# Kernel tuning notes

Measured on AMD Instinct MI355X. Metric: run time of the kernel, lower is better.

The kernel has to match this reference:

```python
import jax, jax.numpy as jnp
import numpy as np

B, H, W, C, S, ITERS = 32, 80, 80, 32, 9, 3
HW = H * W
SCALE = C ** -0.5


def _grid(h, w):
    # matches SoftPositionEmbedding.build_grid: [1, h, w, 4] = [g, 1-g]
    r = jnp.stack(jnp.meshgrid(jnp.linspace(0., 1., h), jnp.linspace(0., 1., w), indexing='ij'), -1)
    return jnp.concatenate([r, 1. - r], -1)[None].astype(jnp.float32)


def _ln(x, g, b, ax):
    m = x.mean(ax, keepdims=True)
    v = x.var(ax, keepdims=True)
    return (x - m) / jnp.sqrt(v + 1e-5) * g + b


def _conv(x, w, b, p):
    y = jax.lax.conv_general_dilated(x, w, (1, 1), [(p, p), (p, p)],
                                     dimension_numbers=('NCHW', 'OIHW', 'NCHW'))
    return y + b[None, :, None, None]


def _convT(x, w, b, p):
    # stride-1 ConvTranspose2d == conv with spatially flipped kernel, pad k-1-p; w is [I,O,kh,kw]
    k = w.shape[-1]
    q = k - 1 - p
    y = jax.lax.conv_general_dilated(x, jnp.flip(w, (2, 3)), (1, 1), [(q, q), (q, q)],
                                     dimension_numbers=('NCHW', 'IOHW', 'NCHW'))
    return y + b[None, :, None, None]


def setup_inputs() -> dict:
    key = jax.random.key(0)
    ks = iter(jax.random.split(key, 64))

    def n(sh, s=0.05):
        return jax.random.normal(next(ks), sh, jnp.float32) * s

    return dict(
        x=jax.random.normal(next(ks), (B, 1, H, W), jnp.float32),
        slot_noise=jax.random.normal(next(ks), (B, S, C), jnp.float32),
        enc_w1=n((C, 1, 5, 5)), enc_b1=jnp.zeros((C,)),
        enc_w2=n((C, C, 5, 5)), enc_b2=jnp.zeros((C,)),
        enc_w3=n((C, C, 5, 5)), enc_b3=jnp.zeros((C,)),
        enc_w4=n((C, C, 5, 5)), enc_b4=jnp.zeros((C,)),
        pe_enc_w=n((C, 4)), pe_enc_b=jnp.zeros((C,)),
        ln_enc_g=jnp.ones((HW, C)), ln_enc_b=jnp.zeros((HW, C)),
        mlp_w1=n((C, C)), mlp_b1=jnp.zeros((C,)),
        mlp_w2=n((C, C)), mlp_b2=jnp.zeros((C,)),
        slots_mu=n((1, 1, C), 1.0), slots_sigma=jnp.abs(n((1, 1, C), 1.0)),
        ni_g=jnp.ones((C,)), ni_b=jnp.zeros((C,)),
        ns_g=jnp.ones((C,)), ns_b=jnp.zeros((C,)),
        q_w=n((C, C)), q_b=jnp.zeros((C,)),
        k_w=n((C, C)), k_b=jnp.zeros((C,)),
        v_w=n((C, C)), v_b=jnp.zeros((C,)),
        gru_wih=n((3 * C, C)), gru_whh=n((3 * C, C)),
        gru_bih=jnp.zeros((3 * C,)), gru_bhh=jnp.zeros((3 * C,)),
        res_ln_g=jnp.ones((C,)), res_ln_b=jnp.zeros((C,)),
        res_w1=n((C, C)), res_b1=jnp.zeros((C,)),
        res_w2=n((C, C)), res_b2=jnp.zeros((C,)),
        pe_dec_w=n((C, 4)), pe_dec_b=jnp.zeros((C,)),
        dec_w1=n((C, C, 5, 5)), dec_b1=jnp.zeros((C,)),
        dec_w2=n((C, C, 5, 5)), dec_b2=jnp.zeros((C,)),
        dec_w3=n((C, C, 5, 5)), dec_b3=jnp.zeros((C,)),
        dec_w4=n((C, 2, 3, 3)), dec_b4=jnp.zeros((2,)),
    )


def _forward(x, slot_noise, enc_w1, enc_b1, enc_w2, enc_b2, enc_w3, enc_b3, enc_w4, enc_b4,
             pe_enc_w, pe_enc_b, ln_enc_g, ln_enc_b, mlp_w1, mlp_b1, mlp_w2, mlp_b2,
             slots_mu, slots_sigma, ni_g, ni_b, ns_g, ns_b, q_w, q_b, k_w, k_b, v_w, v_b,
             gru_wih, gru_whh, gru_bih, gru_bhh, res_ln_g, res_ln_b, res_w1, res_b1,
             res_w2, res_b2, pe_dec_w, pe_dec_b, dec_w1, dec_b1, dec_w2, dec_b2,
             dec_w3, dec_b3, dec_w4, dec_b4):
    grid = _grid(H, W)  # [1,H,W,4]
    # --- conv encoder ---
    h = jax.nn.relu(_conv(x, enc_w1, enc_b1, 2))
    h = jax.nn.relu(_conv(h, enc_w2, enc_b2, 2))
    h = jax.nn.relu(_conv(h, enc_w3, enc_b3, 2))
    h = jax.nn.relu(_conv(h, enc_w4, enc_b4, 2))
    h = h.transpose(0, 2, 3, 1) + (grid @ pe_enc_w.T + pe_enc_b)  # soft pos emb
    h = h.reshape(B, HW, C)
    h = _ln(h, ln_enc_g, ln_enc_b, (-2, -1))  # LayerNorm([HW, C]): joint over last 2 dims
    h = jax.nn.relu(h @ mlp_w1.T + mlp_b1) @ mlp_w2.T + mlp_b2
    # --- slot attention ---
    slots = slots_mu + slots_sigma * slot_noise  # torch.normal(mu, sigma)
    xn = _ln(h, ni_g, ni_b, -1)
    keys = xn @ k_w.T + k_b
    values = xn @ v_w.T + v_b
    attn = None
    for _ in range(ITERS):
        prev = slots
        sn = _ln(slots, ns_g, ns_b, -1)
        q = sn @ q_w.T + q_b
        dots = jnp.einsum('bid,bjd->bij', q, keys) * SCALE  # [B,S,HW]
        attn = jax.nn.softmax(dots, axis=1) + 1e-8  # softmax over slots
        attn = attn / attn.sum(-1, keepdims=True)
        upd = jnp.einsum('bjd,bij->bid', values, attn)  # [B,S,C]
        # PyTorch GRUCell
        u2 = upd.reshape(-1, C)
        h2 = prev.reshape(-1, C)
        gx = u2 @ gru_wih.T + gru_bih
        gh = h2 @ gru_whh.T + gru_bhh
        xr, xz, xc = jnp.split(gx, 3, -1)
        hr, hz, hc = jnp.split(gh, 3, -1)
        r = jax.nn.sigmoid(xr + hr)
        z = jax.nn.sigmoid(xz + hz)
        cand = jnp.tanh(xc + r * hc)
        slots = ((1. - z) * cand + z * h2).reshape(B, S, C)
        res = _ln(slots, res_ln_g, res_ln_b, -1)
        res = jax.nn.relu(res @ res_w1.T + res_b1) @ res_w2.T + res_b2
        slots = slots + res
    # --- spatial-broadcast decoder ---
    d = jnp.broadcast_to(slots.reshape(B * S, 1, 1, C), (B * S, H, W, C))
    d = d + (grid @ pe_dec_w.T + pe_dec_b)
    d = d.transpose(0, 3, 1, 2)
    d = jax.nn.relu(_convT(d, dec_w1, dec_b1, 2))
    d = jax.nn.relu(_convT(d, dec_w2, dec_b2, 2))
    d = jax.nn.relu(_convT(d, dec_w3, dec_b3, 2))
    d = _convT(d, dec_w4, dec_b4, 1)
    d = d.transpose(0, 2, 3, 1).reshape(B, S, H, W, 2)
    recon, mlog = d[..., :1], d[..., 1:]
    mask = jax.nn.softmax(mlog, axis=1)  # over slots
    combined = (recon * mask).sum(1).transpose(0, 3, 1, 2)  # [B,1,H,W]
    return (combined, recon.transpose(0, 1, 4, 2, 3), mask.transpose(0, 1, 4, 2, 3),
            slots, attn.reshape(B, S, 1, H, W))


def reference(x, slot_noise, enc_w1, enc_b1, enc_w2, enc_b2, enc_w3, enc_b3, enc_w4, enc_b4,
              pe_enc_w, pe_enc_b, ln_enc_g, ln_enc_b, mlp_w1, mlp_b1, mlp_w2, mlp_b2,
              slots_mu, slots_sigma, ni_g, ni_b, ns_g, ns_b, q_w, q_b, k_w, k_b, v_w, v_b,
              gru_wih, gru_whh, gru_bih, gru_bhh, res_ln_g, res_ln_b, res_w1, res_b1,
              res_w2, res_b2, pe_dec_w, pe_dec_b, dec_w1, dec_b1, dec_w2, dec_b2,
              dec_w3, dec_b3, dec_w4, dec_b4):
    return _forward(x, slot_noise, enc_w1, enc_b1, enc_w2, enc_b2, enc_w3, enc_b3, enc_w4, enc_b4,
                    pe_enc_w, pe_enc_b, ln_enc_g, ln_enc_b, mlp_w1, mlp_b1, mlp_w2, mlp_b2,
                    slots_mu, slots_sigma, ni_g, ni_b, ns_g, ns_b, q_w, q_b, k_w, k_b, v_w, v_b,
                    gru_wih, gru_whh, gru_bih, gru_bhh, res_ln_g, res_ln_b, res_w1, res_b1,
                    res_w2, res_b2, pe_dec_w, pe_dec_b, dec_w1, dec_b1, dec_w2, dec_b2,
                    dec_w3, dec_b3, dec_w4, dec_b4)
```

## Files before the change

kernel.cpp:

```cpp
#include <hip/hip_runtime.h>
#include <cstddef>
#include <cstdint>


namespace {

constexpr int Bb  = 32;
constexpr int HWp = 6400;
constexpr float SCALEf = 0.17677669529663687f;

constexpr size_t O_COMB  = 0;
constexpr size_t O_RECON = 204800;
constexpr size_t O_MASK  = 2048000;
constexpr size_t O_SLOTS = 3891200;
constexpr size_t O_ATTN  = 3900416;

constexpr size_t W_PEENC = 0;
constexpr size_t W_PEDEC = 204800;
constexpr size_t W_BASE  = 409600;
constexpr size_t W_TC    = 512000;
constexpr size_t W_TS    = 537600;
constexpr size_t W_WP    = 768000;
constexpr size_t W_LNPART= 844800;
constexpr size_t W_MEANR = 846400;
constexpr size_t W_Q     = 846464;
constexpr size_t W_SLOTS = 855680;
constexpr size_t W_APART = 864896;
constexpr size_t W_RSUM  = 872096;
constexpr size_t W_UP2   = 872384;
constexpr size_t W_KEYS  = 1102784;
constexpr size_t W_VALS  = 4379584;
constexpr size_t W_POOL  = 7656384;
constexpr size_t W_TOTAL = 29115328;

typedef __attribute__((ext_vector_type(8))) short short8;
typedef __attribute__((ext_vector_type(4))) float f32x4;

__device__ __forceinline__ ushort f2bf(float f) {
  uint u = __builtin_bit_cast(uint, f);
  uint r = (u + 0x7fffu + ((u >> 16) & 1u)) >> 16;
  return (ushort)r;
}
__device__ __forceinline__ float bf2f(ushort b) {
  uint u = ((uint)b) << 16;
  return __builtin_bit_cast(float, u);
}
__device__ __forceinline__ void unpk2(uint w, float& a, float& b) {
  a = __builtin_bit_cast(float, w << 16);
  b = __builtin_bit_cast(float, w & 0xffff0000u);
}

__device__ __forceinline__ void ln32v(const float* x, const float* __restrict__ g,
                                      const float* __restrict__ b, float* y) {
  float m = 0.f;
#pragma unroll
  for (int c = 0; c < 32; ++c) m += x[c];
  m *= (1.f / 32.f);
  float v = 0.f;
#pragma unroll
  for (int c = 0; c < 32; ++c) { float d = x[c] - m; v += d * d; }
  v *= (1.f / 32.f);
  float rs = rsqrtf(v + 1e-5f);
#pragma unroll
  for (int c = 0; c < 32; ++c) y[c] = (x[c] - m) * rs * g[c] + b[c];
}

__device__ __forceinline__ void matvec32(const float* __restrict__ W,
                                         const float* __restrict__ bias,
                                         const float* x, float* y, bool relu) {
#pragma unroll
  for (int o = 0; o < 32; ++o) {
    float a = bias[o];
#pragma unroll
    for (int c = 0; c < 32; ++c) a = fmaf(x[c], W[o * 32 + c], a);
    y[o] = relu ? fmaxf(a, 0.f) : a;
  }
}

__device__ __forceinline__ float lane_ln(float v, int o, const float* __restrict__ g,
                                         const float* __restrict__ b) {
  float s = v;
#pragma unroll
  for (int m = 16; m >= 1; m >>= 1) s += __shfl_xor(s, m);
  float mean = s * (1.f / 32.f);
  float d = v - mean;
  float q = d * d;
#pragma unroll
  for (int m = 16; m >= 1; m >>= 1) q += __shfl_xor(q, m);
  float rstd = rsqrtf(q * (1.f / 32.f) + 1e-5f);
  return d * rstd * g[o] + b[o];
}


__global__ void k_pe_maps(const float* __restrict__ pew_e, const float* __restrict__ peb_e,
                          const float* __restrict__ pew_d, const float* __restrict__ peb_d,
                          float* __restrict__ pe_enc, float* __restrict__ pe_dec) {
  int hw = blockIdx.x * 256 + threadIdx.x;
  if (hw >= HWp) return;
  int y = hw / 80, x = hw % 80;
  float g0 = y * (1.f / 79.f), g1 = x * (1.f / 79.f);
  float g2 = 1.f - g0, g3 = 1.f - g1;
#pragma unroll
  for (int c = 0; c < 32; ++c) {
    pe_enc[(size_t)hw * 32 + c] = peb_e[c] + g0 * pew_e[c * 4] + g1 * pew_e[c * 4 + 1] +
                                  g2 * pew_e[c * 4 + 2] + g3 * pew_e[c * 4 + 3];
    pe_dec[(size_t)c * HWp + hw] = peb_d[c] + g0 * pew_d[c * 4] + g1 * pew_d[c * 4 + 1] +
                                   g2 * pew_d[c * 4 + 2] + g3 * pew_d[c * 4 + 3];
  }
}


__global__ void k_pack(const float* __restrict__ w, ushort* __restrict__ dst, int trans) {
  int tap = blockIdx.x;
  int grp = threadIdx.x >> 6, lane = threadIdx.x & 63;
  int ky = tap / 5, kx = tap % 5;
  int m = grp * 16 + (lane & 15);
  int kb = (lane >> 4) * 8;
  ushort* o = dst + ((size_t)(tap * 2 + grp) * 64 + lane) * 8;
#pragma unroll
  for (int j = 0; j < 8; ++j) {
    int k = kb + j;
    float v = trans ? w[(size_t)k * 800 + m * 25 + (4 - ky) * 5 + (4 - kx)]
                    : w[(size_t)m * 800 + k * 25 + ky * 5 + kx];
    o[j] = f2bf(v);
  }
}


__global__ void k_prep_tc(const float* __restrict__ w, float* __restrict__ tc) {
  const int rep[5] = {0, 1, 40, 78, 79};
  int cls = blockIdx.x;
  int yc = cls / 5, xc = cls % 5;
  int ci = threadIdx.x >> 5, co = threadIdx.x & 31;
  int yr = rep[yc], xr = rep[xc];
  float s = 0.f;
#pragma unroll
  for (int ky = 0; ky < 5; ++ky) {
    if ((unsigned)(yr + ky - 2) >= 80u) continue;
#pragma unroll
    for (int kx = 0; kx < 5; ++kx) {
      if ((unsigned)(xr + kx - 2) >= 80u) continue;
      s += w[(size_t)ci * 800 + co * 25 + (4 - ky) * 5 + (4 - kx)];
    }
  }
  tc[(size_t)cls * 1024 + ci * 32 + co] = s;
}

__global__ void k_ts(const float* __restrict__ tc, const float* __restrict__ slots,
                     float* __restrict__ ts) {
  int idx = blockIdx.x * 256 + threadIdx.x;
  if (idx >= 288 * 800) return;
  int img = idx / 800, rem = idx % 800;
  int cls = rem >> 5, o = rem & 31;
  float s = 0.f;
#pragma unroll
  for (int ci = 0; ci < 32; ++ci)
    s += tc[(size_t)cls * 1024 + ci * 32 + o] * slots[(size_t)img * 32 + ci];
  ts[idx] = s;
}


template <int MODE, bool RELU>
__global__ __launch_bounds__(256, 2) void k_conv_mfma(
    const void* __restrict__ in_, const ushort* __restrict__ wp,
    const float* __restrict__ bias, ushort* __restrict__ out_,
    const float* __restrict__ ts, int n0) {
  __shared__ int4 sm[4032];
  const int n = blockIdx.y, rt = blockIdx.x;
  const int t = threadIdx.x;

  for (int i = t; i < 4032; i += 256) {
    int x = i % 84, ru = i / 84;
    int r = ru >> 2, u = ru & 3;
    int gy = rt * 8 + r - 2, gx = x - 2;
    int4 pk = {0, 0, 0, 0};
    if ((unsigned)gy < 80u && (unsigned)gx < 80u) {
      int hw = gy * 80 + gx;
      if constexpr (MODE == 0) {
        const float* fp = (const float*)in_;
        ushort bb[8];
#pragma unroll
        for (int j = 0; j < 8; ++j)
          bb[j] = f2bf(fp[(size_t)(u * 8 + j) * HWp + hw]);
        pk.x = (int)((uint)bb[0] | ((uint)bb[1] << 16));
        pk.y = (int)((uint)bb[2] | ((uint)bb[3] << 16));
        pk.z = (int)((uint)bb[4] | ((uint)bb[5] << 16));
        pk.w = (int)((uint)bb[6] | ((uint)bb[7] << 16));
      } else if constexpr (MODE == 1) {
        pk = *(const int4*)((const ushort*)in_ + ((size_t)n * HWp + hw) * 32 + u * 8);
      } else {
        int4 bp = *(const int4*)((const ushort*)in_ + (size_t)hw * 32 + u * 8);
        int yc = gy < 2 ? gy : (gy > 77 ? gy - 75 : 2);
        int xc = gx < 2 ? gx : (gx > 77 ? gx - 75 : 2);
        const float* tp = ts + ((size_t)(n0 + n) * 25 + (yc * 5 + xc)) * 32 + u * 8;
        float t0, t1;
        uint* pw = (uint*)&pk;
        const uint* bw = (const uint*)&bp;
#pragma unroll
        for (int h = 0; h < 4; ++h) {
          unpk2(bw[h], t0, t1);
          float f0 = fmaxf(t0 + tp[2 * h], 0.f);
          float f1 = fmaxf(t1 + tp[2 * h + 1], 0.f);
          pw[h] = (uint)f2bf(f0) | ((uint)f2bf(f1) << 16);
        }
      }
    }
    int up = u ^ ((x >> 1) & 3);
    sm[(r * 84 + x) * 4 + up] = pk;
  }
  __syncthreads();

  const int wv = t >> 6, lane = t & 63;
  const int l15 = lane & 15, lg = lane >> 4;
  const short8* smS = (const short8*)sm;

  f32x4 acc[2][5][2];
#pragma unroll
  for (int a = 0; a < 2; ++a)
#pragma unroll
    for (int b = 0; b < 5; ++b)
#pragma unroll
      for (int c = 0; c < 2; ++c) acc[a][b][c] = f32x4{0.f, 0.f, 0.f, 0.f};

  for (int dy = 0; dy < 5; ++dy) {
    for (int dx = 0; dx < 5; ++dx) {
      int tap = dy * 5 + dx;
      short8 A0 = *(const short8*)(wp + ((size_t)(tap * 2 + 0) * 64 + lane) * 8);
      short8 A1 = *(const short8*)(wp + ((size_t)(tap * 2 + 1) * 64 + lane) * 8);
#pragma unroll
      for (int ri = 0; ri < 2; ++ri) {
        int rbase = (wv * 2 + ri + dy) * 336;
#pragma unroll
        for (int xg = 0; xg < 5; ++xg) {
          int xs = xg * 16 + l15 + dx;
          short8 Bv = smS[rbase + xs * 4 + (lg ^ ((xs >> 1) & 3))];
          acc[ri][xg][0] = __builtin_amdgcn_mfma_f32_16x16x32_bf16(A0, Bv, acc[ri][xg][0], 0, 0, 0);
          acc[ri][xg][1] = __builtin_amdgcn_mfma_f32_16x16x32_bf16(A1, Bv, acc[ri][xg][1], 0, 0, 0);
        }
      }
    }
  }

  float bv[2][4];
#pragma unroll
  for (int cg = 0; cg < 2; ++cg)
#pragma unroll
    for (int q = 0; q < 4; ++q) bv[cg][q] = bias[cg * 16 + lg * 4 + q];
  int y0 = rt * 8 + wv * 2;
#pragma unroll
  for (int ri = 0; ri < 2; ++ri) {
#pragma unroll
    for (int xg = 0; xg < 5; ++xg) {
      size_t px = (size_t)n * HWp + (y0 + ri) * 80 + (xg * 16 + l15);
#pragma unroll
      for (int cg = 0; cg < 2; ++cg) {
        f32x4 v = acc[ri][xg][cg];
        float o0 = v[0] + bv[cg][0], o1 = v[1] + bv[cg][1];
        float o2 = v[2] + bv[cg][2], o3 = v[3] + bv[cg][3];
        if (RELU) {
          o0 = fmaxf(o0, 0.f); o1 = fmaxf(o1, 0.f);
          o2 = fmaxf(o2, 0.f); o3 = fmaxf(o3, 0.f);
        }
        uint2 pk;
        pk.x = (uint)f2bf(o0) | ((uint)f2bf(o1) << 16);
        pk.y = (uint)f2bf(o2) | ((uint)f2bf(o3) << 16);
        *(uint2*)(out_ + px * 32 + cg * 16 + lg * 4) = pk;
      }
    }
  }
}


__global__ __launch_bounds__(256) void k_conv1(const float* __restrict__ in,
                                               const float* __restrict__ w,
                                               const float* __restrict__ b,
                                               ushort* __restrict__ out) {
  int hw = blockIdx.x * 256 + threadIdx.x;
  int n = blockIdx.y;
  int y = hw / 80, x = hw % 80;
  float xv[25];
#pragma unroll
  for (int ky = 0; ky < 5; ++ky)
#pragma unroll
    for (int kx = 0; kx < 5; ++kx) {
      int iy = y + ky - 2, ix = x + kx - 2;
      xv[ky * 5 + kx] = ((unsigned)iy < 80u && (unsigned)ix < 80u)
                            ? in[(size_t)n * HWp + iy * 80 + ix] : 0.f;
    }
  float a[32];
#pragma unroll
  for (int co = 0; co < 32; ++co) {
    float s = b[co];
#pragma unroll
    for (int tp = 0; tp < 25; ++tp) s = fmaf(xv[tp], w[co * 25 + tp], s);
    a[co] = fmaxf(s, 0.f);
  }
  ushort* op = out + ((size_t)n * HWp + hw) * 32;
#pragma unroll
  for (int g = 0; g < 4; ++g) {
    uint4 pk;
    pk.x = (uint)f2bf(a[g * 8 + 0]) | ((uint)f2bf(a[g * 8 + 1]) << 16);
    pk.y = (uint)f2bf(a[g * 8 + 2]) | ((uint)f2bf(a[g * 8 + 3]) << 16);
    pk.z = (uint)f2bf(a[g * 8 + 4]) | ((uint)f2bf(a[g * 8 + 5]) << 16);
    pk.w = (uint)f2bf(a[g * 8 + 6]) | ((uint)f2bf(a[g * 8 + 7]) << 16);
    *(uint4*)(op + g * 8) = pk;
  }
}


__global__ __launch_bounds__(256) void k_conv4(const ushort* __restrict__ in,
                                               const float* __restrict__ w,
                                               const float* __restrict__ b,
                                               float* __restrict__ outR,
                                               float* __restrict__ outM, int n0) {
  __shared__ float sw[2 * 288];
  for (int e = threadIdx.x; e < 576; e += 256) {
    int co = e / 288, rem = e % 288;
    int tap = rem / 32, ci = rem % 32;
    sw[e] = w[(size_t)(ci * 2 + co) * 9 + 8 - tap];
  }
  __syncthreads();
  int hw = blockIdx.x * 256 + threadIdx.x;
  int nl = blockIdx.y;
  int y = hw / 80, x = hw % 80;
  float a0 = b[0], a1 = b[1];
  const ushort* ip = in + (size_t)nl * HWp * 32;
#pragma unroll
  for (int ky = 0; ky < 3; ++ky) {
#pragma unroll
    for (int kx = 0; kx < 3; ++kx) {
      int iy = y + ky - 1, ix = x + kx - 1;
      if ((unsigned)iy >= 80u || (unsigned)ix >= 80u) continue;
      int tap = ky * 3 + kx;
      const int4* p = (const int4*)(ip + (size_t)(iy * 80 + ix) * 32);
      const float* w0 = sw + tap * 32;
      const float* w1 = sw + 288 + tap * 32;
#pragma unroll
      for (int u = 0; u < 4; ++u) {
        int4 ch = p[u];
        const uint* cw = (const uint*)&ch;
#pragma unroll
        for (int h = 0; h < 4; ++h) {
          float v0, v1;
          unpk2(cw[h], v0, v1);
          int ci = u * 8 + h * 2;
          a0 = fmaf(v0, w0[ci], a0);     a1 = fmaf(v0, w1[ci], a1);
          a0 = fmaf(v1, w0[ci + 1], a0); a1 = fmaf(v1, w1[ci + 1], a1);
        }
      }
    }
  }
  outR[(size_t)(n0 + nl) * HWp + hw] = a0;
  outM[(size_t)(n0 + nl) * HWp + hw] = a1;
}


__global__ __launch_bounds__(256) void k_hstats(const ushort* __restrict__ enc,
                                                const float* __restrict__ pe_enc,
                                                float* __restrict__ lnpart) {
  int b = blockIdx.y;
  int hw = blockIdx.x * 256 + threadIdx.x;
  const int4* ep = (const int4*)(enc + ((size_t)b * HWp + hw) * 32);
  float v[32];
#pragma unroll
  for (int u = 0; u < 4; ++u) {
    int4 ch = ep[u];
    const uint* cw = (const uint*)&ch;
#pragma unroll
    for (int h = 0; h < 4; ++h) unpk2(cw[h], v[u * 8 + h * 2], v[u * 8 + h * 2 + 1]);
  }
  float s = 0.f, ss = 0.f;
#pragma unroll
  for (int c = 0; c < 32; ++c) {
    v[c] += pe_enc[(size_t)hw * 32 + c];
    s += v[c]; ss += v[c] * v[c];
  }
  __shared__ float r1[256], r2[256];
  r1[threadIdx.x] = s; r2[threadIdx.x] = ss;
  __syncthreads();
  for (int off = 128; off > 0; off >>= 1) {
    if (threadIdx.x < off) { r1[threadIdx.x] += r1[threadIdx.x + off]; r2[threadIdx.x] += r2[threadIdx.x + off]; }
    __syncthreads();
  }
  if (threadIdx.x == 0) {
    lnpart[(size_t)(b * 25 + blockIdx.x) * 2] = r1[0];
    lnpart[(size_t)(b * 25 + blockIdx.x) * 2 + 1] = r2[0];
  }
}

__global__ void k_statsfin(const float* __restrict__ lnpart, float* __restrict__ meanr) {
  int b = threadIdx.x;
  if (b >= 32) return;
  float s = 0.f, ss = 0.f;
  for (int k = 0; k < 25; ++k) {
    s += lnpart[(size_t)(b * 25 + k) * 2];
    ss += lnpart[(size_t)(b * 25 + k) * 2 + 1];
  }
  float m = s * (1.f / 204800.f);
  float var = ss * (1.f / 204800.f) - m * m;
  meanr[b * 2] = m;
  meanr[b * 2 + 1] = rsqrtf(var + 1e-5f);
}


__global__ __launch_bounds__(256) void k_lnmlpkv(
    const ushort* __restrict__ enc, const float* __restrict__ pe_enc,
    const float* __restrict__ meanr,
    const float* __restrict__ g, const float* __restrict__ bb,
    const float* __restrict__ w1, const float* __restrict__ b1,
    const float* __restrict__ w2, const float* __restrict__ b2,
    const float* __restrict__ nig, const float* __restrict__ nib,
    const float* __restrict__ kw, const float* __restrict__ kb,
    const float* __restrict__ vw, const float* __restrict__ vb,
    ushort* __restrict__ keys, ushort* __restrict__ vals) {
  int b = blockIdx.y;
  int hw = blockIdx.x * 256 + threadIdx.x;
  float x[32], t0[32], t1[32];
  const int4* ep = (const int4*)(enc + ((size_t)b * HWp + hw) * 32);
#pragma unroll
  for (int u = 0; u < 4; ++u) {
    int4 ch = ep[u];
    const uint* cw = (const uint*)&ch;
#pragma unroll
    for (int h = 0; h < 4; ++h) unpk2(cw[h], x[u * 8 + h * 2], x[u * 8 + h * 2 + 1]);
  }
  float m = meanr[b * 2], rs = meanr[b * 2 + 1];
#pragma unroll
  for (int c = 0; c < 32; ++c) {
    float h = x[c] + pe_enc[(size_t)hw * 32 + c];
    x[c] = (h - m) * rs * g[(size_t)hw * 32 + c] + bb[(size_t)hw * 32 + c];
  }
  matvec32(w1, b1, x, t0, true);
  matvec32(w2, b2, t0, t1, false);
  ln32v(t1, nig, nib, x);
  matvec32(kw, kb, x, t0, false);
  matvec32(vw, vb, x, t1, false);
  ushort* kp = keys + ((size_t)b * HWp + hw) * 32;
  ushort* vp = vals + ((size_t)b * HWp + hw) * 32;
#pragma unroll
  for (int gq = 0; gq < 4; ++gq) {
    uint4 pk, pv;
    pk.x = (uint)f2bf(t0[gq * 8 + 0]) | ((uint)f2bf(t0[gq * 8 + 1]) << 16);
    pk.y = (uint)f2bf(t0[gq * 8 + 2]) | ((uint)f2bf(t0[gq * 8 + 3]) << 16);
    pk.z = (uint)f2bf(t0[gq * 8 + 4]) | ((uint)f2bf(t0[gq * 8 + 5]) << 16);
    pk.w = (uint)f2bf(t0[gq * 8 + 6]) | ((uint)f2bf(t0[gq * 8 + 7]) << 16);
    pv.x = (uint)f2bf(t1[gq * 8 + 0]) | ((uint)f2bf(t1[gq * 8 + 1]) << 16);
    pv.y = (uint)f2bf(t1[gq * 8 + 2]) | ((uint)f2bf(t1[gq * 8 + 3]) << 16);
    pv.z = (uint)f2bf(t1[gq * 8 + 4]) | ((uint)f2bf(t1[gq * 8 + 5]) << 16);
    pv.w = (uint)f2bf(t1[gq * 8 + 6]) | ((uint)f2bf(t1[gq * 8 + 7]) << 16);
    *(uint4*)(kp + gq * 8) = pk;
    *(uint4*)(vp + gq * 8) = pv;
  }
}


__global__ __launch_bounds__(256) void k_init_q(
    const float* __restrict__ mu, const float* __restrict__ sig,
    const float* __restrict__ noise,
    const float* __restrict__ nsg, const float* __restrict__ nsb,
    const float* __restrict__ qw, const float* __restrict__ qb,
    float* __restrict__ slots, float* __restrict__ qbuf) {
  int rl = threadIdx.x >> 5, o = threadIdx.x & 31;
  int r = blockIdx.x * 8 + rl;
  float s = mu[o] + sig[o] * noise[(size_t)r * 32 + o];
  slots[(size_t)r * 32 + o] = s;
  float y = lane_ln(s, o, nsg, nsb);
  __shared__ float S[8][32];
  S[rl][o] = y;
  __syncthreads();
  float qv = qb[o];
#pragma unroll
  for (int c = 0; c < 32; ++c) qv = fmaf(S[rl][c], qw[o * 32 + c], qv);
  qbuf[(size_t)r * 32 + o] = qv;
}

template <bool LAST>
__global__ __launch_bounds__(256) void k_dots_upd(
    const float* __restrict__ qbuf, const ushort* __restrict__ keys,
    const ushort* __restrict__ vals, float* __restrict__ attnt,
    float* __restrict__ apart, float* __restrict__ up2) {
  int b = blockIdx.y, jb = blockIdx.x;
  int t = threadIdx.x;
  int j = jb * 256 + t;
  __shared__ float qs[288];
  __shared__ float aL[2304];
  __shared__ float wr[36];
  for (int e = t; e < 288; e += 256) qs[e] = qbuf[(size_t)b * 288 + e];
  __syncthreads();
  float k[32];
  const int4* kp = (const int4*)(keys + ((size_t)b * HWp + j) * 32);
#pragma unroll
  for (int u = 0; u < 4; ++u) {
    int4 ch = kp[u];
    const uint* cw = (const uint*)&ch;
#pragma unroll
    for (int h = 0; h < 4; ++h) unpk2(cw[h], k[u * 8 + h * 2], k[u * 8 + h * 2 + 1]);
  }
  float d[9];
#pragma unroll
  for (int i = 0; i < 9; ++i) {
    float a = 0.f;
#pragma unroll
    for (int c = 0; c < 32; ++c) a = fmaf(qs[i * 32 + c], k[c], a);
    d[i] = a * SCALEf;
  }
  float mx = d[0];
#pragma unroll
  for (int i = 1; i < 9; ++i) mx = fmaxf(mx, d[i]);
  float sum = 0.f;
#pragma unroll
  for (int i = 0; i < 9; ++i) { d[i] = __expf(d[i] - mx); sum += d[i]; }
  float inv = 1.f / sum;
  float a9[9];
#pragma unroll
  for (int i = 0; i < 9; ++i) {
    a9[i] = d[i] * inv + 1e-8f;
    if (LAST) attnt[((size_t)b * 9 + i) * HWp + j] = a9[i];
    aL[t * 9 + i] = a9[i];
  }
  int lane = t & 63, wid = t >> 6;
#pragma unroll
  for (int i = 0; i < 9; ++i) {
    float v = a9[i];
    for (int off = 32; off > 0; off >>= 1) v += __shfl_down(v, off);
    if (lane == 0) wr[wid * 9 + i] = v;
  }
  __syncthreads();
  if (t < 9)
    apart[(size_t)(b * 9 + t) * 25 + jb] = wr[t] + wr[9 + t] + wr[18 + t] + wr[27 + t];
  int c = t & 31, g = t >> 5;
  float acc[9];
#pragma unroll
  for (int i = 0; i < 9; ++i) acc[i] = 0.f;
  const ushort* vp = vals + ((size_t)b * HWp + jb * 256) * 32 + c;
  for (int jj = g; jj < 256; jj += 8) {
    float v = bf2f(vp[(size_t)jj * 32]);
#pragma unroll
    for (int i = 0; i < 9; ++i) acc[i] = fmaf(v, aL[jj * 9 + i], acc[i]);
  }
  __syncthreads();
#pragma unroll
  for (int i = 0; i < 9; ++i) aL[(i * 8 + g) * 32 + c] = acc[i];
  __syncthreads();
  for (int i = g; i < 9; i += 8) {
    float s = 0.f;
#pragma unroll
    for (int g2 = 0; g2 < 8; ++g2) s += aL[(i * 8 + g2) * 32 + c];
    up2[(((size_t)b * 25 + jb) * 9 + i) * 32 + c] = s;
  }
}

__global__ __launch_bounds__(256) void k_gru_fused(
    const float* __restrict__ up2, const float* __restrict__ apart,
    float* __restrict__ slots, float* __restrict__ rowsum, float* __restrict__ qbuf,
    const float* __restrict__ wih, const float* __restrict__ whh,
    const float* __restrict__ bih, const float* __restrict__ bhh,
    const float* __restrict__ rlg, const float* __restrict__ rlb,
    const float* __restrict__ rw1, const float* __restrict__ rb1,
    const float* __restrict__ rw2, const float* __restrict__ rb2,
    const float* __restrict__ nsg, const float* __restrict__ nsb,
    const float* __restrict__ qw, const float* __restrict__ qb) {
  int rl = threadIdx.x >> 5, o = threadIdx.x & 31;
  int r = blockIdx.x * 8 + rl;
  int b = r / 9, i = r - b * 9;

  float rs = 0.f;
#pragma unroll
  for (int k = 0; k < 25; ++k) rs += apart[(size_t)(b * 9 + i) * 25 + k];
  if (o == 0) rowsum[r] = rs;

  float uo = 0.f;
#pragma unroll
  for (int jc = 0; jc < 25; ++jc) uo += up2[(((size_t)b * 25 + jc) * 9 + i) * 32 + o];
  uo /= rs;
  float ho = slots[(size_t)r * 32 + o];

  __shared__ float Us[8][32], Hs[8][32];
  Us[rl][o] = uo; Hs[rl][o] = ho;
  __syncthreads();

  float xr = bih[o], xz = bih[32 + o], xc = bih[64 + o];
  float hr = bhh[o], hz = bhh[32 + o], hc = bhh[64 + o];
#pragma unroll
  for (int c = 0; c < 32; ++c) {
    float u = Us[rl][c], h = Hs[rl][c];
    xr = fmaf(u, wih[o * 32 + c], xr);          hr = fmaf(h, whh[o * 32 + c], hr);
    xz = fmaf(u, wih[(32 + o) * 32 + c], xz);   hz = fmaf(h, whh[(32 + o) * 32 + c], hz);
    xc = fmaf(u, wih[(64 + o) * 32 + c], xc);   hc = fmaf(h, whh[(64 + o) * 32 + c], hc);
  }
  float rr = 1.f / (1.f + __expf(-(xr + hr)));
  float zz = 1.f / (1.f + __expf(-(xz + hz)));
  float cand = tanhf(xc + rr * hc);
  float sm = (1.f - zz) * cand + zz * ho;

  float y = lane_ln(sm, o, rlg, rlb);
  __syncthreads();
  Us[rl][o] = y;
  __syncthreads();
  float t1 = rb1[o];
#pragma unroll
  for (int c = 0; c < 32; ++c) t1 = fmaf(Us[rl][c], rw1[o * 32 + c], t1);
  t1 = fmaxf(t1, 0.f);
  Hs[rl][o] = t1;
  __syncthreads();
  float res = rb2[o];
#pragma unroll
  for (int c = 0; c < 32; ++c) res = fmaf(Hs[rl][c], rw2[o * 32 + c], res);
  float ns = sm + res;
  slots[(size_t)r * 32 + o] = ns;

  float y2 = lane_ln(ns, o, nsg, nsb);
  __syncthreads();
  Us[rl][o] = y2;
  __syncthreads();
  float qv = qb[o];
#pragma unroll
  for (int c = 0; c < 32; ++c) qv = fmaf(Us[rl][c], qw[o * 32 + c], qv);
  qbuf[(size_t)r * 32 + o] = qv;
}


__global__ void k_attn_out(const float* __restrict__ attnt, const float* __restrict__ rsum,
                           float* __restrict__ out) {
  size_t idx = (size_t)blockIdx.x * 256 + threadIdx.x;
  out[O_ATTN + idx] = attnt[idx] / rsum[idx / HWp];
}

__global__ void k_slots_out(const float* __restrict__ slots, float* __restrict__ out) {
  int idx = blockIdx.x * 256 + threadIdx.x;
  if (idx < 9216) out[O_SLOTS + idx] = slots[idx];
}

__global__ __launch_bounds__(256) void k_final(float* __restrict__ out) {
  int b = blockIdx.y;
  int j = blockIdx.x * 256 + threadIdx.x;
  float r[9], ml[9];
#pragma unroll
  for (int s = 0; s < 9; ++s) {
    r[s]  = out[O_RECON + (size_t)(b * 9 + s) * HWp + j];
    ml[s] = out[O_MASK  + (size_t)(b * 9 + s) * HWp + j];
  }
  float mx = ml[0];
#pragma unroll
  for (int s = 1; s < 9; ++s) mx = fmaxf(mx, ml[s]);
  float sum = 0.f;
#pragma unroll
  for (int s = 0; s < 9; ++s) { ml[s] = __expf(ml[s] - mx); sum += ml[s]; }
  float inv = 1.f / sum;
  float comb = 0.f;
#pragma unroll
  for (int s = 0; s < 9; ++s) {
    float mk = ml[s] * inv;
    comb = fmaf(r[s], mk, comb);
    out[O_MASK + (size_t)(b * 9 + s) * HWp + j] = mk;
  }
  out[O_COMB + (size_t)b * HWp + j] = comb;
}

}


extern "C" void kernel_launch(void* const* d_in, const int* in_sizes, int n_in,
                              void* d_out, int out_size, void* d_ws, size_t ws_size,
                              hipStream_t stream) {
  if (ws_size < W_TOTAL * sizeof(float)) return;

  const float* in_x       = (const float*)d_in[0];
  const float* slot_noise = (const float*)d_in[1];
  const float* enc_w1 = (const float*)d_in[2];   const float* enc_b1 = (const float*)d_in[3];
  const float* enc_w2 = (const float*)d_in[4];   const float* enc_b2 = (const float*)d_in[5];
  const float* enc_w3 = (const float*)d_in[6];   const float* enc_b3 = (const float*)d_in[7];
  const float* enc_w4 = (const float*)d_in[8];   const float* enc_b4 = (const float*)d_in[9];
  const float* pe_enc_w = (const float*)d_in[10]; const float* pe_enc_b = (const float*)d_in[11];
  const float* ln_enc_g = (const float*)d_in[12]; const float* ln_enc_b = (const float*)d_in[13];
  const float* mlp_w1 = (const float*)d_in[14];  const float* mlp_b1 = (const float*)d_in[15];
  const float* mlp_w2 = (const float*)d_in[16];  const float* mlp_b2 = (const float*)d_in[17];
  const float* slots_mu = (const float*)d_in[18]; const float* slots_sigma = (const float*)d_in[19];
  const float* ni_g = (const float*)d_in[20];    const float* ni_b = (const float*)d_in[21];
  const float* ns_g = (const float*)d_in[22];    const float* ns_b = (const float*)d_in[23];
  const float* q_w = (const float*)d_in[24];     const float* q_b = (const float*)d_in[25];
  const float* k_w = (const float*)d_in[26];     const float* k_b = (const float*)d_in[27];
  const float* v_w = (const float*)d_in[28];     const float* v_b = (const float*)d_in[29];
  const float* gru_wih = (const float*)d_in[30]; const float* gru_whh = (const float*)d_in[31];
  const float* gru_bih = (const float*)d_in[32]; const float* gru_bhh = (const float*)d_in[33];
  const float* res_ln_g = (const float*)d_in[34]; const float* res_ln_b = (const float*)d_in[35];
  const float* res_w1 = (const float*)d_in[36];  const float* res_b1 = (const float*)d_in[37];
  const float* res_w2 = (const float*)d_in[38];  const float* res_b2 = (const float*)d_in[39];
  const float* pe_dec_w = (const float*)d_in[40]; const float* pe_dec_b = (const float*)d_in[41];
  const float* dec_w1 = (const float*)d_in[42];  const float* dec_b1 = (const float*)d_in[43];
  const float* dec_w2 = (const float*)d_in[44];  const float* dec_b2 = (const float*)d_in[45];
  const float* dec_w3 = (const float*)d_in[46];  const float* dec_b3 = (const float*)d_in[47];
  const float* dec_w4 = (const float*)d_in[48];  const float* dec_b4 = (const float*)d_in[49];

  float* ws  = (float*)d_ws;
  float* out = (float*)d_out;
  ushort* wp = (ushort*)(ws + W_WP);

  k_pe_maps<<<dim3(25), 256, 0, stream>>>(pe_enc_w, pe_enc_b, pe_dec_w, pe_dec_b,
                                          ws + W_PEENC, ws + W_PEDEC);

  const size_t WPSTR = 25 * 2 * 64 * 8;
  k_pack<<<dim3(25), 128, 0, stream>>>(enc_w2, wp + 0 * WPSTR, 0);
  k_pack<<<dim3(25), 128, 0, stream>>>(enc_w3, wp + 1 * WPSTR, 0);
  k_pack<<<dim3(25), 128, 0, stream>>>(enc_w4, wp + 2 * WPSTR, 0);
  k_pack<<<dim3(25), 128, 0, stream>>>(dec_w1, wp + 3 * WPSTR, 1);
  k_pack<<<dim3(25), 128, 0, stream>>>(dec_w2, wp + 4 * WPSTR, 1);
  k_pack<<<dim3(25), 128, 0, stream>>>(dec_w3, wp + 5 * WPSTR, 1);
  k_prep_tc<<<dim3(25), 1024, 0, stream>>>(dec_w1, ws + W_TC);

  ushort* base  = (ushort*)(ws + W_BASE);
  ushort* keys  = (ushort*)(ws + W_KEYS);
  ushort* vals  = (ushort*)(ws + W_VALS);
  float*  attnt = ws + W_POOL;
  ushort* E1    = (ushort*)(ws + W_POOL);
  ushort* E2    = (ushort*)(ws + W_POOL + 3276800);

  k_conv_mfma<0, false><<<dim3(10, 1), 256, 0, stream>>>(
      ws + W_PEDEC, wp + 3 * WPSTR, dec_b1, base, nullptr, 0);

  k_conv1<<<dim3(25, Bb), 256, 0, stream>>>(in_x, enc_w1, enc_b1, E1);
  k_conv_mfma<1, true><<<dim3(10, Bb), 256, 0, stream>>>(E1, wp + 0 * WPSTR, enc_b2, E2, nullptr, 0);
  k_conv_mfma<1, true><<<dim3(10, Bb), 256, 0, stream>>>(E2, wp + 1 * WPSTR, enc_b3, E1, nullptr, 0);
  k_conv_mfma<1, true><<<dim3(10, Bb), 256, 0, stream>>>(E1, wp + 2 * WPSTR, enc_b4, E2, nullptr, 0);

  k_hstats<<<dim3(25, Bb), 256, 0, stream>>>(E2, ws + W_PEENC, ws + W_LNPART);
  k_statsfin<<<dim3(1), 64, 0, stream>>>(ws + W_LNPART, ws + W_MEANR);
  k_lnmlpkv<<<dim3(25, Bb), 256, 0, stream>>>(E2, ws + W_PEENC, ws + W_MEANR,
                                              ln_enc_g, ln_enc_b,
                                              mlp_w1, mlp_b1, mlp_w2, mlp_b2,
                                              ni_g, ni_b, k_w, k_b, v_w, v_b,
                                              keys, vals);

  k_init_q<<<dim3(36), 256, 0, stream>>>(slots_mu, slots_sigma, slot_noise,
                                         ns_g, ns_b, q_w, q_b, ws + W_SLOTS, ws + W_Q);
  for (int it = 0; it < 3; ++it) {
    if (it == 2)
      k_dots_upd<true><<<dim3(25, Bb), 256, 0, stream>>>(ws + W_Q, keys, vals, attnt,
                                                         ws + W_APART, ws + W_UP2);
    else
      k_dots_upd<false><<<dim3(25, Bb), 256, 0, stream>>>(ws + W_Q, keys, vals, attnt,
                                                          ws + W_APART, ws + W_UP2);
    k_gru_fused<<<dim3(36), 256, 0, stream>>>(ws + W_UP2, ws + W_APART,
                                              ws + W_SLOTS, ws + W_RSUM, ws + W_Q,
                                              gru_wih, gru_whh, gru_bih, gru_bhh,
                                              res_ln_g, res_ln_b, res_w1, res_b1,
                                              res_w2, res_b2, ns_g, ns_b, q_w, q_b);
  }
  k_attn_out<<<dim3(7200), 256, 0, stream>>>(attnt, ws + W_RSUM, out);
  k_slots_out<<<dim3(36), 256, 0, stream>>>(ws + W_SLOTS, out);

  k_ts<<<dim3(900), 256, 0, stream>>>(ws + W_TC, ws + W_SLOTS, ws + W_TS);

  ushort* XA = (ushort*)(ws + W_POOL);
  ushort* XB = XA + (size_t)96 * 32 * HWp;
  for (int ch = 0; ch < 3; ++ch) {
    int n0 = ch * 96;
    k_conv_mfma<2, true><<<dim3(10, 96), 256, 0, stream>>>(base, wp + 4 * WPSTR, dec_b2, XA,
                                                           ws + W_TS, n0);
    k_conv_mfma<1, true><<<dim3(10, 96), 256, 0, stream>>>(XA, wp + 5 * WPSTR, dec_b3, XB,
                                                           nullptr, 0);
    k_conv4<<<dim3(25, 96), 256, 0, stream>>>(XB, dec_w4, dec_b4,
                                              out + O_RECON, out + O_MASK, n0);
  }

  k_final<<<dim3(25, Bb), 256, 0, stream>>>(out);
}
```

Baseline: 696.9 us.

## Run encoder LN+MLP+K/V projection on MFMA bf16 matrix cores

Replaces the per-thread scalar fp32 matvec chain (MLP two layers, LayerNorm, K and V projections) with bf16 MFMA 16x16x32 ops. The four 32x32 weights are pre-packed into MFMA fragment layout, and intermediates go through swizzled LDS to re-layout between layers. LayerNorm is done with cross-lane shuffles. This cuts the heavy scalar FMA and register cost of the old kernel. The tradeoff is extra bf16 rounding of intermediate activations.

```diff
diff --git a/kernel.cpp b/kernel.cpp
--- a/kernel.cpp
+++ b/kernel.cpp
@@ -21,16 +21,17 @@
 constexpr size_t W_TC    = 512000;
 constexpr size_t W_TS    = 537600;
 constexpr size_t W_WP    = 768000;
-constexpr size_t W_LNPART= 844800;
-constexpr size_t W_MEANR = 846400;
-constexpr size_t W_Q     = 846464;
-constexpr size_t W_SLOTS = 855680;
-constexpr size_t W_APART = 864896;
-constexpr size_t W_RSUM  = 872096;
-constexpr size_t W_UP2   = 872384;
-constexpr size_t W_KEYS  = 1102784;
-constexpr size_t W_VALS  = 4379584;
-constexpr size_t W_POOL  = 7656384;
+constexpr size_t W_WPM   = 844800;
+constexpr size_t W_LNPART= 846848;
+constexpr size_t W_MEANR = 848448;
+constexpr size_t W_Q     = 848512;
+constexpr size_t W_SLOTS = 857728;
+constexpr size_t W_APART = 866944;
+constexpr size_t W_RSUM  = 874144;
+constexpr size_t W_UP2   = 874432;
+constexpr size_t W_KEYS  = 1104832;
+constexpr size_t W_VALS  = 4381632;
+constexpr size_t W_POOL  = 7658432;
 constexpr size_t W_TOTAL = 29115328;
 
 typedef __attribute__((ext_vector_type(8))) short short8;
@@ -48,21 +49,6 @@
 __device__ __forceinline__ void unpk2(uint w, float& a, float& b) {
   a = __builtin_bit_cast(float, w << 16);
   b = __builtin_bit_cast(float, w & 0xffff0000u);
-}
-
-__device__ __forceinline__ void ln32v(const float* x, const float* __restrict__ g,
-                                      const float* __restrict__ b, float* y) {
-  float m = 0.f;
-#pragma unroll
-  for (int c = 0; c < 32; ++c) m += x[c];
-  m *= (1.f / 32.f);
-  float v = 0.f;
-#pragma unroll
-  for (int c = 0; c < 32; ++c) { float d = x[c] - m; v += d * d; }
-  v *= (1.f / 32.f);
-  float rs = rsqrtf(v + 1e-5f);
-#pragma unroll
-  for (int c = 0; c < 32; ++c) y[c] = (x[c] - m) * rs * g[c] + b[c];
 }
 
 __device__ __forceinline__ void matvec32(const float* __restrict__ W,
@@ -124,6 +110,14 @@
                     : w[(size_t)m * 800 + k * 25 + ky * 5 + kx];
     o[j] = f2bf(v);
   }
+}
+
+__global__ void k_pack_mat(const float* __restrict__ w, ushort* __restrict__ dst) {
+  int grp = threadIdx.x >> 6, lane = threadIdx.x & 63;
+  int m = grp * 16 + (lane & 15), kb = (lane >> 4) * 8;
+  ushort* o = dst + ((size_t)(grp * 64 + lane)) * 8;
+#pragma unroll
+  for (int j = 0; j < 8; ++j) o[j] = f2bf(w[m * 32 + kb + j]);
 }
 
 
@@ -403,53 +397,155 @@
 }
 
 
-__global__ __launch_bounds__(256) void k_lnmlpkv(
-    const ushort* __restrict__ enc, const float* __restrict__ pe_enc,
+__global__ __launch_bounds__(256) void k_lnmlpkv_mfma(
+    const ushort* __restrict__ enc, const float* __restrict__ pe,
     const float* __restrict__ meanr,
     const float* __restrict__ g, const float* __restrict__ bb,
-    const float* __restrict__ w1, const float* __restrict__ b1,
-    const float* __restrict__ w2, const float* __restrict__ b2,
+    const ushort* __restrict__ wm,
+    const float* __restrict__ b1, const float* __restrict__ b2,
     const float* __restrict__ nig, const float* __restrict__ nib,
-    const float* __restrict__ kw, const float* __restrict__ kb,
-    const float* __restrict__ vw, const float* __restrict__ vb,
+    const float* __restrict__ kb, const float* __restrict__ vb,
     ushort* __restrict__ keys, ushort* __restrict__ vals) {
-  int b = blockIdx.y;
-  int hw = blockIdx.x * 256 + threadIdx.x;
-  float x[32], t0[32], t1[32];
-  const int4* ep = (const int4*)(enc + ((size_t)b * HWp + hw) * 32);
-#pragma unroll
-  for (int u = 0; u < 4; ++u) {
-    int4 ch = ep[u];
-    const uint* cw = (const uint*)&ch;
-#pragma unroll
-    for (int h = 0; h < 4; ++h) unpk2(cw[h], x[u * 8 + h * 2], x[u * 8 + h * 2 + 1]);
-  }
-  float m = meanr[b * 2], rs = meanr[b * 2 + 1];
-#pragma unroll
-  for (int c = 0; c < 32; ++c) {
-    float h = x[c] + pe_enc[(size_t)hw * 32 + c];
-    x[c] = (h - m) * rs * g[(size_t)hw * 32 + c] + bb[(size_t)hw * 32 + c];
-  }
-  matvec32(w1, b1, x, t0, true);
-  matvec32(w2, b2, t0, t1, false);
-  ln32v(t1, nig, nib, x);
-  matvec32(kw, kb, x, t0, false);
-  matvec32(vw, vb, x, t1, false);
-  ushort* kp = keys + ((size_t)b * HWp + hw) * 32;
-  ushort* vp = vals + ((size_t)b * HWp + hw) * 32;
-#pragma unroll
-  for (int gq = 0; gq < 4; ++gq) {
-    uint4 pk, pv;
-    pk.x = (uint)f2bf(t0[gq * 8 + 0]) | ((uint)f2bf(t0[gq * 8 + 1]) << 16);
-    pk.y = (uint)f2bf(t0[gq * 8 + 2]) | ((uint)f2bf(t0[gq * 8 + 3]) << 16);
-    pk.z = (uint)f2bf(t0[gq * 8 + 4]) | ((uint)f2bf(t0[gq * 8 + 5]) << 16);
-    pk.w = (uint)f2bf(t0[gq * 8 + 6]) | ((uint)f2bf(t0[gq * 8 + 7]) << 16);
-    pv.x = (uint)f2bf(t1[gq * 8 + 0]) | ((uint)f2bf(t1[gq * 8 + 1]) << 16);
-    pv.y = (uint)f2bf(t1[gq * 8 + 2]) | ((uint)f2bf(t1[gq * 8 + 3]) << 16);
-    pv.z = (uint)f2bf(t1[gq * 8 + 4]) | ((uint)f2bf(t1[gq * 8 + 5]) << 16);
-    pv.w = (uint)f2bf(t1[gq * 8 + 6]) | ((uint)f2bf(t1[gq * 8 + 7]) << 16);
-    *(uint4*)(kp + gq * 8) = pk;
-    *(uint4*)(vp + gq * 8) = pv;
+  __shared__ ushort ls[256 * 32];
+  const int b = blockIdx.y, jb = blockIdx.x;
+  const int t = threadIdx.x, wv = t >> 6, lane = t & 63;
+  const int l15 = lane & 15, lg = lane >> 4;
+  const int skey = l15 & 3;
+
+  short8 A[4][2];
+#pragma unroll
+  for (int mt = 0; mt < 4; ++mt)
+#pragma unroll
+    for (int gr = 0; gr < 2; ++gr)
+      A[mt][gr] = *(const short8*)(wm + ((size_t)(mt * 2 + gr) * 64 + lane) * 8);
+
+  float4 b1v0 = *(const float4*)(b1 + lg * 4),  b1v1 = *(const float4*)(b1 + 16 + lg * 4);
+  float4 b2v0 = *(const float4*)(b2 + lg * 4),  b2v1 = *(const float4*)(b2 + 16 + lg * 4);
+  float4 ng0  = *(const float4*)(nig + lg * 4), ng1  = *(const float4*)(nig + 16 + lg * 4);
+  float4 nb0  = *(const float4*)(nib + lg * 4), nb1  = *(const float4*)(nib + 16 + lg * 4);
+  float4 kbv0 = *(const float4*)(kb + lg * 4),  kbv1 = *(const float4*)(kb + 16 + lg * 4);
+  float4 vbv0 = *(const float4*)(vb + lg * 4),  vbv1 = *(const float4*)(vb + 16 + lg * 4);
+
+  const float m_ = meanr[b * 2], rs_ = meanr[b * 2 + 1];
+
+  short8 bx[4];
+#pragma unroll
+  for (int g2 = 0; g2 < 4; ++g2) {
+    int pos = jb * 256 + wv * 64 + g2 * 16 + l15;
+    int4 e = *(const int4*)(enc + ((size_t)b * HWp + pos) * 32 + lg * 8);
+    float xv[8];
+    const uint* ew = (const uint*)&e;
+#pragma unroll
+    for (int h = 0; h < 4; ++h) unpk2(ew[h], xv[2 * h], xv[2 * h + 1]);
+    float4 p0 = *(const float4*)(pe + (size_t)pos * 32 + lg * 8);
+    float4 p1 = *(const float4*)(pe + (size_t)pos * 32 + lg * 8 + 4);
+    float4 g0 = *(const float4*)(g + (size_t)pos * 32 + lg * 8);
+    float4 g1 = *(const float4*)(g + (size_t)pos * 32 + lg * 8 + 4);
+    float4 q0 = *(const float4*)(bb + (size_t)pos * 32 + lg * 8);
+    float4 q1 = *(const float4*)(bb + (size_t)pos * 32 + lg * 8 + 4);
+    float pv[8] = {p0.x, p0.y, p0.z, p0.w, p1.x, p1.y, p1.z, p1.w};
+    float gv[8] = {g0.x, g0.y, g0.z, g0.w, g1.x, g1.y, g1.z, g1.w};
+    float qv[8] = {q0.x, q0.y, q0.z, q0.w, q1.x, q1.y, q1.z, q1.w};
+    uint pk[4];
+#pragma unroll
+    for (int h = 0; h < 4; ++h) {
+      float f0 = (xv[2 * h] + pv[2 * h] - m_) * rs_ * gv[2 * h] + qv[2 * h];
+      float f1 = (xv[2 * h + 1] + pv[2 * h + 1] - m_) * rs_ * gv[2 * h + 1] + qv[2 * h + 1];
+      pk[h] = (uint)f2bf(f0) | ((uint)f2bf(f1) << 16);
+    }
+    bx[g2] = __builtin_bit_cast(short8, *(int4*)pk);
+  }
+
+  auto lds_write = [&](int posl, int cg, const f32x4& v) {
+    int u = cg * 2 + (lg >> 1);
+    int us = u ^ skey;
+    uint2 pk;
+    pk.x = (uint)f2bf(v[0]) | ((uint)f2bf(v[1]) << 16);
+    pk.y = (uint)f2bf(v[2]) | ((uint)f2bf(v[3]) << 16);
+    *(uint2*)(ls + (size_t)posl * 32 + us * 8 + (lg & 1) * 4) = pk;
+  };
+
+#pragma unroll
+  for (int g2 = 0; g2 < 4; ++g2) {
+    int posl = wv * 64 + g2 * 16 + l15;
+    f32x4 a0 = __builtin_amdgcn_mfma_f32_16x16x32_bf16(A[0][0], bx[g2], f32x4{0, 0, 0, 0}, 0, 0, 0);
+    f32x4 a1 = __builtin_amdgcn_mfma_f32_16x16x32_bf16(A[0][1], bx[g2], f32x4{0, 0, 0, 0}, 0, 0, 0);
+    f32x4 r0, r1;
+#pragma unroll
+    for (int q = 0; q < 4; ++q) {
+      r0[q] = fmaxf(a0[q] + (&b1v0.x)[q], 0.f);
+      r1[q] = fmaxf(a1[q] + (&b1v1.x)[q], 0.f);
+    }
+    lds_write(posl, 0, r0);
+    lds_write(posl, 1, r1);
+  }
+  __syncthreads();
+  short8 t0f[4];
+#pragma unroll
+  for (int g2 = 0; g2 < 4; ++g2) {
+    int posl = wv * 64 + g2 * 16 + l15;
+    t0f[g2] = *(const short8*)(ls + (size_t)posl * 32 + (lg ^ skey) * 8);
+  }
+  __syncthreads();
+
+#pragma unroll
+  for (int g2 = 0; g2 < 4; ++g2) {
+    int posl = wv * 64 + g2 * 16 + l15;
+    f32x4 c0 = __builtin_amdgcn_mfma_f32_16x16x32_bf16(A[1][0], t0f[g2], f32x4{0, 0, 0, 0}, 0, 0, 0);
+    f32x4 c1 = __builtin_amdgcn_mfma_f32_16x16x32_bf16(A[1][1], t0f[g2], f32x4{0, 0, 0, 0}, 0, 0, 0);
+#pragma unroll
+    for (int q = 0; q < 4; ++q) { c0[q] += (&b2v0.x)[q]; c1[q] += (&b2v1.x)[q]; }
+    float s = 0.f;
+#pragma unroll
+    for (int q = 0; q < 4; ++q) s += c0[q] + c1[q];
+    s += __shfl_xor(s, 16); s += __shfl_xor(s, 32);
+    float mean = s * (1.f / 32.f);
+    float var = 0.f;
+#pragma unroll
+    for (int q = 0; q < 4; ++q) {
+      float d0 = c0[q] - mean, d1 = c1[q] - mean;
+      var += d0 * d0 + d1 * d1;
+    }
+    var += __shfl_xor(var, 16); var += __shfl_xor(var, 32);
+    float rstd = rsqrtf(var * (1.f / 32.f) + 1e-5f);
+    f32x4 y0, y1;
+#pragma unroll
+    for (int q = 0; q < 4; ++q) {
+      y0[q] = (c0[q] - mean) * rstd * (&ng0.x)[q] + (&nb0.x)[q];
+      y1[q] = (c1[q] - mean) * rstd * (&ng1.x)[q] + (&nb1.x)[q];
+    }
+    lds_write(posl, 0, y0);
+    lds_write(posl, 1, y1);
+  }
+  __syncthreads();
+  short8 xnf[4];
+#pragma unroll
+  for (int g2 = 0; g2 < 4; ++g2) {
+    int posl = wv * 64 + g2 * 16 + l15;
+    xnf[g2] = *(const short8*)(ls + (size_t)posl * 32 + (lg ^ skey) * 8);
+  }
+
+#pragma unroll
+  for (int g2 = 0; g2 < 4; ++g2) {
+    int pos = jb * 256 + wv * 64 + g2 * 16 + l15;
+    size_t px = ((size_t)b * HWp + pos) * 32;
+    f32x4 k0 = __builtin_amdgcn_mfma_f32_16x16x32_bf16(A[2][0], xnf[g2], f32x4{0, 0, 0, 0}, 0, 0, 0);
+    f32x4 k1 = __builtin_amdgcn_mfma_f32_16x16x32_bf16(A[2][1], xnf[g2], f32x4{0, 0, 0, 0}, 0, 0, 0);
+    f32x4 v0 = __builtin_amdgcn_mfma_f32_16x16x32_bf16(A[3][0], xnf[g2], f32x4{0, 0, 0, 0}, 0, 0, 0);
+    f32x4 v1 = __builtin_amdgcn_mfma_f32_16x16x32_bf16(A[3][1], xnf[g2], f32x4{0, 0, 0, 0}, 0, 0, 0);
+    uint2 pk;
+    pk.x = (uint)f2bf(k0[0] + kbv0.x) | ((uint)f2bf(k0[1] + kbv0.y) << 16);
+    pk.y = (uint)f2bf(k0[2] + kbv0.z) | ((uint)f2bf(k0[3] + kbv0.w) << 16);
+    *(uint2*)(keys + px + lg * 4) = pk;
+    pk.x = (uint)f2bf(k1[0] + kbv1.x) | ((uint)f2bf(k1[1] + kbv1.y) << 16);
+    pk.y = (uint)f2bf(k1[2] + kbv1.z) | ((uint)f2bf(k1[3] + kbv1.w) << 16);
+    *(uint2*)(keys + px + 16 + lg * 4) = pk;
+    pk.x = (uint)f2bf(v0[0] + vbv0.x) | ((uint)f2bf(v0[1] + vbv0.y) << 16);
+    pk.y = (uint)f2bf(v0[2] + vbv0.z) | ((uint)f2bf(v0[3] + vbv0.w) << 16);
+    *(uint2*)(vals + px + lg * 4) = pk;
+    pk.x = (uint)f2bf(v1[0] + vbv1.x) | ((uint)f2bf(v1[1] + vbv1.y) << 16);
+    pk.y = (uint)f2bf(v1[2] + vbv1.z) | ((uint)f2bf(v1[3] + vbv1.w) << 16);
+    *(uint2*)(vals + px + 16 + lg * 4) = pk;
   }
 }
 
@@ -694,7 +790,8 @@
 
   float* ws  = (float*)d_ws;
   float* out = (float*)d_out;
-  ushort* wp = (ushort*)(ws + W_WP);
+  ushort* wp  = (ushort*)(ws + W_WP);
+  ushort* wpm = (ushort*)(ws + W_WPM);
 
   k_pe_maps<<<dim3(25), 256, 0, stream>>>(pe_enc_w, pe_enc_b, pe_dec_w, pe_dec_b,
                                           ws + W_PEENC, ws + W_PEDEC);
@@ -706,6 +803,10 @@
   k_pack<<<dim3(25), 128, 0, stream>>>(dec_w1, wp + 3 * WPSTR, 1);
   k_pack<<<dim3(25), 128, 0, stream>>>(dec_w2, wp + 4 * WPSTR, 1);
   k_pack<<<dim3(25), 128, 0, stream>>>(dec_w3, wp + 5 * WPSTR, 1);
+  k_pack_mat<<<dim3(1), 128, 0, stream>>>(mlp_w1, wpm + 0 * 1024);
+  k_pack_mat<<<dim3(1), 128, 0, stream>>>(mlp_w2, wpm + 1 * 1024);
+  k_pack_mat<<<dim3(1), 128, 0, stream>>>(k_w,   wpm + 2 * 1024);
+  k_pack_mat<<<dim3(1), 128, 0, stream>>>(v_w,   wpm + 3 * 1024);
   k_prep_tc<<<dim3(25), 1024, 0, stream>>>(dec_w1, ws + W_TC);
 
   ushort* base  = (ushort*)(ws + W_BASE);
@@ -725,11 +826,10 @@
 
   k_hstats<<<dim3(25, Bb), 256, 0, stream>>>(E2, ws + W_PEENC, ws + W_LNPART);
   k_statsfin<<<dim3(1), 64, 0, stream>>>(ws + W_LNPART, ws + W_MEANR);
-  k_lnmlpkv<<<dim3(25, Bb), 256, 0, stream>>>(E2, ws + W_PEENC, ws + W_MEANR,
-                                              ln_enc_g, ln_enc_b,
-                                              mlp_w1, mlp_b1, mlp_w2, mlp_b2,
-                                              ni_g, ni_b, k_w, k_b, v_w, v_b,
-                                              keys, vals);
+  k_lnmlpkv_mfma<<<dim3(25, Bb), 256, 0, stream>>>(E2, ws + W_PEENC, ws + W_MEANR,
+                                                   ln_enc_g, ln_enc_b, wpm,
+                                                   mlp_b1, mlp_b2, ni_g, ni_b,
+                                                   k_b, v_b, keys, vals);
 
   k_init_q<<<dim3(36), 256, 0, stream>>>(slots_mu, slots_sigma, slot_noise,
                                          ns_g, ns_b, q_w, q_b, ws + W_SLOTS, ws + W_Q);
```

Result: faster. 637.0 us (-8.6%).
